# Kernel optimization log

Hardware: AMD Instinct MI355X
Metric: run time of the kernel (lower is better)

## Reference

```python
import jax, jax.numpy as jnp
import numpy as np

B, L, K = 4, 1024, 48
EF, NF, NPE, NRBF, NCLS = 128, 128, 16, 16, 3
MAXREL = 32
EDGE_IN = NPE + NRBF * 25  # 416


def setup_inputs():
    key = jax.random.key(0)
    ks = jax.random.split(key, 8)
    X = jax.random.normal(ks[0], (B, L, 4, 3), jnp.float32)
    mask = jnp.ones((B, L), jnp.float32)
    R_idx = jnp.arange(B * L, dtype=jnp.int64).reshape(B, L)
    chain_labels = jax.random.randint(ks[1], (B, L), 0, 4).astype(jnp.int64)
    membrane_per_residue_labels = jax.random.randint(ks[2], (B, L), 0, NCLS).astype(jnp.int64)
    pe_w = jax.random.normal(ks[3], (2 * MAXREL + 2, NPE), jnp.float32) * 0.05
    pe_b = jax.random.normal(ks[4], (NPE,), jnp.float32) * 0.05
    edge_w = jax.random.normal(ks[5], (EDGE_IN, EF), jnp.float32) * 0.05
    ne_g = jnp.ones((EF,), jnp.float32)
    ne_b = jnp.zeros((EF,), jnp.float32)
    node_w = jax.random.normal(ks[6], (NCLS, NF), jnp.float32) * 0.05
    nn_g = jnp.ones((NF,), jnp.float32)
    nn_b = jnp.zeros((NF,), jnp.float32)
    return {"X": X, "mask": mask, "R_idx": R_idx, "chain_labels": chain_labels,
            "membrane_per_residue_labels": membrane_per_residue_labels,
            "pe_w": pe_w, "pe_b": pe_b, "edge_w": edge_w, "ne_g": ne_g, "ne_b": ne_b,
            "node_w": node_w, "nn_g": nn_g, "nn_b": nn_b}


def _rbf(D):
    mu = jnp.linspace(2.0, 22.0, NRBF)
    sigma = (22.0 - 2.0) / NRBF
    return jnp.exp(-(((D[..., None] - mu) / sigma) ** 2))


def _gather_nb(v, e_idx):
    # v: [B, L, ...] -> [B, L, K, ...] gathered along residue dim
    return jax.vmap(lambda vi, ii: vi[ii])(v, e_idx)


def _ln(x, g, b, eps=1e-5):
    mu = jnp.mean(x, -1, keepdims=True)
    var = jnp.mean((x - mu) ** 2, -1, keepdims=True)
    return (x - mu) / jnp.sqrt(var + eps) * g + b


# 24 atom-pair RBFs after the Ca-Ca (D_neighbors) one, in the original concat order
PAIRS = [("N","N"),("C","C"),("O","O"),("Cb","Cb"),("Ca","N"),("Ca","C"),("Ca","O"),
         ("Ca","Cb"),("N","C"),("N","O"),("N","Cb"),("Cb","C"),("Cb","O"),("O","C"),
         ("N","Ca"),("C","Ca"),("O","Ca"),("Cb","Ca"),("C","N"),("O","N"),("Cb","N"),
         ("C","Cb"),("O","Cb"),("C","O")]


def reference(X, mask, R_idx, chain_labels, membrane_per_residue_labels,
              pe_w, pe_b, edge_w, ne_g, ne_b, node_w, nn_g, nn_b):
    Na, Ca, Cc, Oo = X[:, :, 0], X[:, :, 1], X[:, :, 2], X[:, :, 3]
    bvec = Ca - Na
    cvec = Cc - Ca
    avec = jnp.cross(bvec, cvec)
    Cb = -0.58273431 * avec + 0.56802827 * bvec - 0.54067466 * cvec + Ca
    coords = {"N": Na, "Ca": Ca, "C": Cc, "O": Oo, "Cb": Cb}

    # masked Ca-Ca distances + kNN (single NxN pass)
    mask2 = mask[:, :, None] * mask[:, None, :]
    dX = Ca[:, :, None, :] - Ca[:, None, :, :]
    D = mask2 * jnp.sqrt(jnp.sum(dX ** 2, -1) + 1e-6)
    D_max = jnp.max(D, -1, keepdims=True)
    D_adj = D + (1.0 - mask2) * D_max
    negD, E_idx = jax.lax.top_k(-D_adj, K)
    D_neighbors = -negD  # [B, L, K]

    # gather neighbor coords once, compute the 25 RBF features on N*K pairs only
    nb = {n: _gather_nb(v, E_idx) for n, v in coords.items()}  # [B, L, K, 3]
    rbf_list = [_rbf(D_neighbors)]
    for an, bn in PAIRS:
        d = jnp.sqrt(jnp.sum((coords[an][:, :, None, :] - nb[bn]) ** 2, -1) + 1e-6)
        rbf_list.append(_rbf(d))
    RBF_all = jnp.concatenate(rbf_list, -1)  # [B, L, K, 400]

    # positional encodings on gathered offsets / chain equality
    off = R_idx[:, :, None] - _gather_nb(R_idx, E_idx)           # [B, L, K]
    E_chains = (chain_labels[:, :, None] == _gather_nb(chain_labels, E_idx)).astype(jnp.int32)
    d = jnp.clip(off + MAXREL, 0, 2 * MAXREL).astype(jnp.int32) * E_chains + (1 - E_chains) * (2 * MAXREL + 1)
    d1h = jax.nn.one_hot(d, 2 * MAXREL + 2, dtype=jnp.float32)
    E_pos = d1h @ pe_w + pe_b                                     # [B, L, K, 16]

    E = jnp.concatenate([E_pos, RBF_all], -1) @ edge_w            # [B, L, K, 128]
    E = _ln(E, ne_g, ne_b)

    C1h = jax.nn.one_hot(membrane_per_residue_labels, NCLS, dtype=jnp.float32)
    V = _ln(C1h @ node_w, nn_g, nn_b)                             # [B, L, 128]
    return V, E, E_idx
```

## Files before the change

### kernel.cpp

```cpp
#include <hip/hip_runtime.h>
#include <math.h>

#define B_ 4
#define L_ 1024
#define K_ 48
#define EF_ 128
#define NF_ 128
#define NPE_ 16
#define NRBF_ 16
#define MAXREL_ 32
#define EDGE_IN_ 416

#define V_SIZE   (B_*L_*NF_)
#define E_OFF    (V_SIZE)
#define E_SIZE   (B_*L_*K_*EF_)
#define EIDX_OFF (E_OFF + E_SIZE)

#define XH4_STRIDE 136

typedef __attribute__((ext_vector_type(8))) short bf16x8;
typedef __attribute__((ext_vector_type(4))) float f32x4;
typedef __attribute__((ext_vector_type(4))) unsigned u32x4;

__device__ const int PA_[25] = {1, 0,2,3,4, 1,1,1,1, 0,0,0, 4,4, 3, 0,2,3,4, 2,3,4, 2,3, 2};
__device__ const int PB_[25] = {1, 0,2,3,4, 0,2,3,4, 2,3,4, 2,3, 2, 1,1,1,1, 0,0,0, 4,4, 3};

__device__ __forceinline__ unsigned short f2bf(float f){
    unsigned u = __float_as_uint(f);
    unsigned r = u + 0x7fffu + ((u >> 16) & 1u);
    return (unsigned short)(r >> 16);
}

__device__ __forceinline__ float pair_dist(const float* sAI, const float (*sAJ)[16], int e, int g2) {
    float dx = sAI[PA_[g2]*3+0] - sAJ[e][PB_[g2]*3+0];
    float dy = sAI[PA_[g2]*3+1] - sAJ[e][PB_[g2]*3+1];
    float dz = sAI[PA_[g2]*3+2] - sAJ[e][PB_[g2]*3+2];
    return sqrtf(dx*dx + dy*dy + dz*dz + 1e-6f);
}

__device__ __forceinline__ void rbf16(unsigned short* dst, float dist) {
    float t = 0.8f * dist - 1.6f;
    unsigned pk[8];
    #pragma unroll
    for (int rr = 0; rr < 8; ++rr) {
        float v0 = __expf(-t * t); t -= 1.06666672f;
        float v1 = __expf(-t * t); t -= 1.06666672f;
        asm("v_cvt_pk_bf16_f32 %0, %1, %2" : "=v"(pk[rr]) : "v"(v0), "v"(v1));
    }
    u32x4 w0 = {pk[0], pk[1], pk[2], pk[3]};
    u32x4 w1 = {pk[4], pk[5], pk[6], pk[7]};
    *(u32x4*)dst = w0;
    *(u32x4*)(dst + 8) = w1;
}

template<int NG, int GF, int CB>
__device__ __forceinline__ void rbf_quarter(unsigned short* xh, const float* sAI,
                                            const float (*sAJ)[16], int tid) {
    for (int idx = tid; idx < K_ * NG; idx += 256) {
        int e = idx / NG, g = idx - e * NG;
        rbf16(&xh[e * XH4_STRIDE + CB + g * 16], pair_dist(sAI, sAJ, e, GF + g));
    }
}

template<int NKS, int KB>
__device__ __forceinline__ void mfma_quarter(f32x4 (&acc)[3][2], const unsigned short* xh,
                                             const unsigned short* w0p, const unsigned short* w1p,
                                             int lr, int lg) {
    #pragma unroll
    for (int ks = 0; ks < NKS; ++ks) {
        int k0 = ks * 32;
        bf16x8 a0, a1, a2, wb0, wb1;
        wb0 = *(const bf16x8*)(w0p + KB + k0);
        wb1 = *(const bf16x8*)(w1p + KB + k0);
        a0 = *(const bf16x8*)&xh[(lr)      * XH4_STRIDE + k0 + lg*8];
        a1 = *(const bf16x8*)&xh[(16 + lr) * XH4_STRIDE + k0 + lg*8];
        a2 = *(const bf16x8*)&xh[(32 + lr) * XH4_STRIDE + k0 + lg*8];
        acc[0][0] = __builtin_amdgcn_mfma_f32_16x16x32_bf16(a0, wb0, acc[0][0], 0, 0, 0);
        acc[0][1] = __builtin_amdgcn_mfma_f32_16x16x32_bf16(a0, wb1, acc[0][1], 0, 0, 0);
        acc[1][0] = __builtin_amdgcn_mfma_f32_16x16x32_bf16(a1, wb0, acc[1][0], 0, 0, 0);
        acc[1][1] = __builtin_amdgcn_mfma_f32_16x16x32_bf16(a1, wb1, acc[1][1], 0, 0, 0);
        acc[2][0] = __builtin_amdgcn_mfma_f32_16x16x32_bf16(a2, wb0, acc[2][0], 0, 0, 0);
        acc[2][1] = __builtin_amdgcn_mfma_f32_16x16x32_bf16(a2, wb1, acc[2][1], 0, 0, 0);
    }
}

__global__ __launch_bounds__(256) void wprep_kernel(const float* __restrict__ w,
                                                    unsigned short* __restrict__ wt)
{
    int idx = blockIdx.x * 256 + threadIdx.x;
    if (idx >= EDGE_IN_ * EF_) return;
    int f = idx & 127;
    int k = idx >> 7;
    wt[f * EDGE_IN_ + k] = f2bf(w[k * EF_ + f]);
}

__global__ __launch_bounds__(128) void v_kernel(const int* __restrict__ labels,
                                                const float* __restrict__ node_w,
                                                const float* __restrict__ g,
                                                const float* __restrict__ bb,
                                                float* __restrict__ out)
{
    int gi = blockIdx.x;
    int f  = threadIdx.x;
    int lbl = labels[gi];
    float v = node_w[lbl*NF_ + f];

    __shared__ float red[2];
    __shared__ float red2[2];
    float s = v;
    #pragma unroll
    for (int m = 1; m < 64; m <<= 1) s += __shfl_xor(s, m, 64);
    if ((f & 63) == 0) red[f >> 6] = s;
    __syncthreads();
    float mu = (red[0] + red[1]) * (1.0f / NF_);
    float d = v - mu;
    float s2 = d * d;
    #pragma unroll
    for (int m = 1; m < 64; m <<= 1) s2 += __shfl_xor(s2, m, 64);
    if ((f & 63) == 0) red2[f >> 6] = s2;
    __syncthreads();
    float var = (red2[0] + red2[1]) * (1.0f / NF_);
    out[gi*NF_ + f] = d * rsqrtf(var + 1e-5f) * g[f] + bb[f];
}

__global__ __launch_bounds__(256, 7) void fused_kernel(const float* __restrict__ X,
                                                   const float* __restrict__ mask,
                                                   const int* __restrict__ Ridx,
                                                   const int* __restrict__ chains,
                                                   const float* __restrict__ pe_w,
                                                   const float* __restrict__ pe_b,
                                                   const unsigned short* __restrict__ wt,
                                                   const float* __restrict__ ne_g,
                                                   const float* __restrict__ ne_b,
                                                   float* __restrict__ out)
{
    __shared__ __align__(16) unsigned char sBuf[16384];
    __shared__ __align__(16) unsigned char sAux[1536];
    __shared__ float sAI[16];
    __shared__ float sAJ[K_][16];
    __shared__ int   sJ[K_];
    __shared__ int   sDpos[K_];

    float* sCa = (float*)sBuf;
    float* sM  = (float*)(sBuf + 12288);
    unsigned short* xh = (unsigned short*)sBuf;

    unsigned long long* cand = (unsigned long long*)sAux;
    unsigned* hist   = (unsigned*)(sAux + 384);
    float*    wmax   = (float*)(sAux + 1408);
    int*      sSelBin= (int*)(sAux + 1424);
    unsigned* sSelLo = (unsigned*)(sAux + 1428);
    unsigned* sCnt   = (unsigned*)(sAux + 1432);
    float* stats  = (float*)sAux;
    float* stats2 = (float*)(sAux + 768);

    int tid = threadIdx.x;
    int gi  = blockIdx.x;
    int b   = gi >> 10;
    int i   = gi & (L_ - 1);

    for (int idx = tid; idx < L_ * 3; idx += 256) {
        int j = idx / 3, d = idx - j * 3;
        sCa[idx] = X[(((size_t)((b << 10) + j)) * 4 + 1) * 3 + d];
    }
    for (int j = tid; j < L_; j += 256) sM[j] = mask[(b << 10) + j];
    if (tid == 0) *sCnt = 0;
    __syncthreads();

    float cx = sCa[i*3+0], cy = sCa[i*3+1], cz = sCa[i*3+2];
    float mi = sM[i];

    float dist4[4], m2r[4];
    float lmax = 0.0f;
    #pragma unroll
    for (int q = 0; q < 4; ++q) {
        int j = tid + q * 256;
        float dx = cx - sCa[j*3+0];
        float dy = cy - sCa[j*3+1];
        float dz = cz - sCa[j*3+2];
        float dist = sqrtf(dx*dx + dy*dy + dz*dz + 1e-6f);
        float m2 = mi * sM[j];
        dist4[q] = dist; m2r[q] = m2;
        lmax = fmaxf(lmax, m2 * dist);
    }
    #pragma unroll
    for (int m = 1; m < 64; m <<= 1) lmax = fmaxf(lmax, __shfl_xor(lmax, m, 64));
    if ((tid & 63) == 0) wmax[tid >> 6] = lmax;
    __syncthreads();
    float Dmax = fmaxf(fmaxf(wmax[0], wmax[1]), fmaxf(wmax[2], wmax[3]));

    unsigned long long key[4];
    bool act[4];
    #pragma unroll
    for (int q = 0; q < 4; ++q) {
        int j = tid + q * 256;
        float Dadj = m2r[q] * dist4[q] + (1.0f - m2r[q]) * Dmax;
        key[q] = (((unsigned long long)__float_as_uint(Dadj)) << 32) | (unsigned)j;
        act[q] = true;
    }

    unsigned r = K_ - 1;
    unsigned long long T = 0;
    const int shifts[6] = {56, 48, 40, 32, 8, 0};
    #pragma unroll 1
    for (int p = 0; p < 6; ++p) {
        int sh = shifts[p];
        hist[tid] = 0;
        __syncthreads();
        #pragma unroll
        for (int q = 0; q < 4; ++q)
            if (act[q]) atomicAdd(&hist[(unsigned)((key[q] >> sh) & 255ULL)], 1u);
        __syncthreads();
        if (tid < 64) {
            unsigned b0 = hist[tid*4+0], b1 = hist[tid*4+1], b2 = hist[tid*4+2], b3 = hist[tid*4+3];
            unsigned s0 = b0, s1 = s0 + b1, s2 = s1 + b2, s3 = s2 + b3;
            unsigned s = s3;
            #pragma unroll
            for (int m = 1; m < 64; m <<= 1) {
                unsigned o = __shfl_up(s, m, 64);
                if (tid >= m) s += o;
            }
            unsigned base = s - s3;
            hist[tid*4+0] = base + s0;
            hist[tid*4+1] = base + s1;
            hist[tid*4+2] = base + s2;
            hist[tid*4+3] = base + s3;
        }
        __syncthreads();
        unsigned lo = (tid == 0) ? 0u : hist[tid - 1];
        unsigned hi = hist[tid];
        if (r >= lo && r < hi) { *sSelBin = tid; *sSelLo = lo; }
        __syncthreads();
        int bsel = *sSelBin;
        r -= *sSelLo;
        T |= ((unsigned long long)(unsigned)bsel) << sh;
        #pragma unroll
        for (int q = 0; q < 4; ++q)
            act[q] = act[q] && ((unsigned)((key[q] >> sh) & 255ULL) == (unsigned)bsel);
        __syncthreads();
    }

    #pragma unroll
    for (int q = 0; q < 4; ++q)
        if (key[q] <= T) {
            unsigned pos = atomicAdd(sCnt, 1u);
            cand[pos] = key[q];
        }
    __syncthreads();

    if (tid < 64) {
        unsigned long long k64 = (tid < K_) ? cand[tid] : 0xffffffffffffffffULL;
        #pragma unroll
        for (unsigned kk = 2; kk <= 64; kk <<= 1) {
            #pragma unroll
            for (unsigned jj = kk >> 1; jj > 0; jj >>= 1) {
                unsigned long long o = __shfl_xor(k64, jj, 64);
                bool lower = (tid & jj) == 0;
                bool asc   = (tid & kk) == 0;
                unsigned long long mn = (k64 < o) ? k64 : o;
                unsigned long long mx = (k64 < o) ? o : k64;
                k64 = (lower == asc) ? mn : mx;
            }
        }
        if (tid < K_) {
            int j = (int)(unsigned)(k64 & 0xffffffffULL);
            sJ[tid] = j;
            out[EIDX_OFF + (size_t)gi * K_ + tid] = (float)j;
        }
    }
    __syncthreads();

    if (tid < K_ + 1) {
        int rr = (tid < K_) ? sJ[tid] : i;
        const float* xr = X + ((size_t)((b << 10) + rr)) * 12;
        float n0=xr[0],  n1=xr[1],  n2=xr[2];
        float a0=xr[3],  a1=xr[4],  a2=xr[5];
        float c0=xr[6],  c1=xr[7],  c2=xr[8];
        float o0=xr[9],  o1=xr[10], o2=xr[11];
        float bx=a0-n0, by=a1-n1, bz=a2-n2;
        float vx=c0-a0, vy=c1-a1, vz=c2-a2;
        float ax = by*vz - bz*vy;
        float ay = bz*vx - bx*vz;
        float az = bx*vy - by*vx;
        float cb0 = -0.58273431f*ax + 0.56802827f*bx - 0.54067466f*vx + a0;
        float cb1 = -0.58273431f*ay + 0.56802827f*by - 0.54067466f*vy + a1;
        float cb2 = -0.58273431f*az + 0.56802827f*bz - 0.54067466f*vz + a2;
        float* dst = (tid < K_) ? &sAJ[tid][0] : &sAI[0];
        dst[0]=n0;  dst[1]=n1;  dst[2]=n2;
        dst[3]=a0;  dst[4]=a1;  dst[5]=a2;
        dst[6]=c0;  dst[7]=c1;  dst[8]=c2;
        dst[9]=o0;  dst[10]=o1; dst[11]=o2;
        dst[12]=cb0; dst[13]=cb1; dst[14]=cb2;
    }
    if (tid >= 64 && tid < 64 + K_) {
        int e = tid - 64;
        int j = sJ[e];
        int off  = Ridx[gi] - Ridx[(b << 10) + j];
        int same = (chains[gi] == chains[(b << 10) + j]);
        int dcl = off + MAXREL_;
        dcl = dcl < 0 ? 0 : (dcl > 2*MAXREL_ ? 2*MAXREL_ : dcl);
        sDpos[e] = same ? dcl : (2*MAXREL_ + 1);
    }
    __syncthreads();

    const int wv = tid >> 6;
    const int ln = tid & 63;
    const int lr = ln & 15;
    const int lg = ln >> 4;

    f32x4 acc[3][2];
    #pragma unroll
    for (int rf = 0; rf < 3; ++rf)
        #pragma unroll
        for (int cf = 0; cf < 2; ++cf)
            acc[rf][cf] = (f32x4){0.0f, 0.0f, 0.0f, 0.0f};

    const unsigned short* wbase0 = wt + (size_t)(wv*32 + lr) * EDGE_IN_ + lg*8;
    const unsigned short* wbase1 = wt + (size_t)(wv*32 + 16 + lr) * EDGE_IN_ + lg*8;

    #pragma unroll
    for (int p = 0; p < 2; ++p) {
        int idx = tid + p * 256;
        if (idx < 384) {
            int e = idx >> 3, cc = (idx & 7) * 2;
            int dp = sDpos[e];
            float v0 = pe_w[dp*NPE_ + cc]     + pe_b[cc];
            float v1 = pe_w[dp*NPE_ + cc + 1] + pe_b[cc + 1];
            unsigned pk;
            asm("v_cvt_pk_bf16_f32 %0, %1, %2" : "=v"(pk) : "v"(v0), "v"(v1));
            *(unsigned*)&xh[e * XH4_STRIDE + cc] = pk;
        }
    }
    rbf_quarter<7, 0, 16>(xh, sAI, sAJ, tid);
    __syncthreads();
    mfma_quarter<4, 0>(acc, xh, wbase0, wbase1, lr, lg);
    __syncthreads();
    rbf_quarter<6, 7, 0>(xh, sAI, sAJ, tid);
    __syncthreads();
    mfma_quarter<3, 128>(acc, xh, wbase0, wbase1, lr, lg);
    __syncthreads();
    rbf_quarter<6, 13, 0>(xh, sAI, sAJ, tid);
    __syncthreads();
    mfma_quarter<3, 224>(acc, xh, wbase0, wbase1, lr, lg);
    __syncthreads();
    rbf_quarter<6, 19, 0>(xh, sAI, sAJ, tid);
    __syncthreads();
    mfma_quarter<3, 320>(acc, xh, wbase0, wbase1, lr, lg);

    #pragma unroll
    for (int rf = 0; rf < 3; ++rf)
        #pragma unroll
        for (int r4 = 0; r4 < 4; ++r4) {
            float v0 = acc[rf][0][r4], v1 = acc[rf][1][r4];
            float s  = v0 + v1;
            float s2 = v0*v0 + v1*v1;
            #pragma unroll
            for (int m = 1; m < 16; m <<= 1) {
                s  += __shfl_xor(s,  m, 64);
                s2 += __shfl_xor(s2, m, 64);
            }
            if (lr == 0) {
                int row = rf*16 + lg*4 + r4;
                stats [wv*K_ + row] = s;
                stats2[wv*K_ + row] = s2;
            }
        }
    __syncthreads();

    int colg = wv*32 + lr;
    float gv0 = ne_g[colg],      bv0 = ne_b[colg];
    float gv1 = ne_g[colg + 16], bv1 = ne_b[colg + 16];

    #pragma unroll
    for (int rf = 0; rf < 3; ++rf)
        #pragma unroll
        for (int r4 = 0; r4 < 4; ++r4) {
            int row = rf*16 + lg*4 + r4;
            float sum = stats [row] + stats [K_ + row] + stats [2*K_ + row] + stats [3*K_ + row];
            float sq  = stats2[row] + stats2[K_ + row] + stats2[2*K_ + row] + stats2[3*K_ + row];
            float mu   = sum * (1.0f / 128.0f);
            float var  = sq * (1.0f / 128.0f) - mu * mu;
            float rstd = rsqrtf(var + 1e-5f);
            float* dst = out + E_OFF + (size_t)(gi * K_ + row) * EF_ + colg;
            __builtin_nontemporal_store((acc[rf][0][r4] - mu) * rstd * gv0 + bv0, dst);
            __builtin_nontemporal_store((acc[rf][1][r4] - mu) * rstd * gv1 + bv1, dst + 16);
        }
}

extern "C" void kernel_launch(void* const* d_in, const int* in_sizes, int n_in,
                              void* d_out, int out_size, void* d_ws, size_t ws_size,
                              hipStream_t stream)
{
    const float* X      = (const float*)d_in[0];
    const float* mask   = (const float*)d_in[1];
    const int*   Ridx   = (const int*)d_in[2];
    const int*   chains = (const int*)d_in[3];
    const int*   memb   = (const int*)d_in[4];
    const float* pe_w   = (const float*)d_in[5];
    const float* pe_b   = (const float*)d_in[6];
    const float* edge_w = (const float*)d_in[7];
    const float* ne_g   = (const float*)d_in[8];
    const float* ne_b   = (const float*)d_in[9];
    const float* node_w = (const float*)d_in[10];
    const float* nn_g   = (const float*)d_in[11];
    const float* nn_b   = (const float*)d_in[12];
    float* out = (float*)d_out;

    unsigned short* wt = (unsigned short*)d_ws;

    wprep_kernel<<<(EDGE_IN_*EF_ + 255)/256, 256, 0, stream>>>(edge_w, wt);
    v_kernel<<<B_*L_, 128, 0, stream>>>(memb, node_w, nn_g, nn_b, out);
    fused_kernel<<<B_*L_, 256, 0, stream>>>(X, mask, Ridx, chains, pe_w, pe_b,
                                            wt, ne_g, ne_b, out);
}
```

Before: 110.0 us.

## Single-pass 12-bit histogram top-K select and two-half RBF/MFMA staging

```diff
diff --git a/kernel.cpp b/kernel.cpp
--- a/kernel.cpp
+++ b/kernel.cpp
@@ -16,7 +16,7 @@
 #define E_SIZE   (B_*L_*K_*EF_)
 #define EIDX_OFF (E_OFF + E_SIZE)
 
-#define XH4_STRIDE 136
+#define XH_STRIDE 232
 
 typedef __attribute__((ext_vector_type(8))) short bf16x8;
 typedef __attribute__((ext_vector_type(4))) float f32x4;
@@ -53,28 +53,19 @@
     *(u32x4*)(dst + 8) = w1;
 }
 
-template<int NG, int GF, int CB>
-__device__ __forceinline__ void rbf_quarter(unsigned short* xh, const float* sAI,
-                                            const float (*sAJ)[16], int tid) {
-    for (int idx = tid; idx < K_ * NG; idx += 256) {
-        int e = idx / NG, g = idx - e * NG;
-        rbf16(&xh[e * XH4_STRIDE + CB + g * 16], pair_dist(sAI, sAJ, e, GF + g));
-    }
-}
-
 template<int NKS, int KB>
-__device__ __forceinline__ void mfma_quarter(f32x4 (&acc)[3][2], const unsigned short* xh,
-                                             const unsigned short* w0p, const unsigned short* w1p,
-                                             int lr, int lg) {
+__device__ __forceinline__ void mfma_half(f32x4 (&acc)[3][2], const unsigned short* xh,
+                                          const unsigned short* w0p, const unsigned short* w1p,
+                                          int lr, int lg) {
     #pragma unroll
     for (int ks = 0; ks < NKS; ++ks) {
         int k0 = ks * 32;
         bf16x8 a0, a1, a2, wb0, wb1;
         wb0 = *(const bf16x8*)(w0p + KB + k0);
         wb1 = *(const bf16x8*)(w1p + KB + k0);
-        a0 = *(const bf16x8*)&xh[(lr)      * XH4_STRIDE + k0 + lg*8];
-        a1 = *(const bf16x8*)&xh[(16 + lr) * XH4_STRIDE + k0 + lg*8];
-        a2 = *(const bf16x8*)&xh[(32 + lr) * XH4_STRIDE + k0 + lg*8];
+        a0 = *(const bf16x8*)&xh[(lr)      * XH_STRIDE + k0 + lg*8];
+        a1 = *(const bf16x8*)&xh[(16 + lr) * XH_STRIDE + k0 + lg*8];
+        a2 = *(const bf16x8*)&xh[(32 + lr) * XH_STRIDE + k0 + lg*8];
         acc[0][0] = __builtin_amdgcn_mfma_f32_16x16x32_bf16(a0, wb0, acc[0][0], 0, 0, 0);
         acc[0][1] = __builtin_amdgcn_mfma_f32_16x16x32_bf16(a0, wb1, acc[0][1], 0, 0, 0);
         acc[1][0] = __builtin_amdgcn_mfma_f32_16x16x32_bf16(a1, wb0, acc[1][0], 0, 0, 0);
@@ -123,7 +114,7 @@
     out[gi*NF_ + f] = d * rsqrtf(var + 1e-5f) * g[f] + bb[f];
 }
 
-__global__ __launch_bounds__(256, 7) void fused_kernel(const float* __restrict__ X,
+__global__ __launch_bounds__(256, 5) void fused_kernel(const float* __restrict__ X,
                                                    const float* __restrict__ mask,
                                                    const int* __restrict__ Ridx,
                                                    const int* __restrict__ chains,
@@ -134,25 +125,24 @@
                                                    const float* __restrict__ ne_b,
                                                    float* __restrict__ out)
 {
-    __shared__ __align__(16) unsigned char sBuf[16384];
-    __shared__ __align__(16) unsigned char sAux[1536];
+    __shared__ __align__(16) unsigned char sBuf[K_ * XH_STRIDE * 2];
     __shared__ float sAI[16];
     __shared__ float sAJ[K_][16];
     __shared__ int   sJ[K_];
     __shared__ int   sDpos[K_];
+    __shared__ unsigned long long cand[64];
+    __shared__ float stats [4 * K_];
+    __shared__ float stats2[4 * K_];
+    __shared__ float wmax[4];
+    __shared__ unsigned wsum[4];
+    __shared__ int sSelBin;
+    __shared__ unsigned sSelLo, sSelCnt, sCnt;
+    __shared__ unsigned long long sTkey;
 
     float* sCa = (float*)sBuf;
     float* sM  = (float*)(sBuf + 12288);
+    unsigned* hist32 = (unsigned*)sBuf;
     unsigned short* xh = (unsigned short*)sBuf;
-
-    unsigned long long* cand = (unsigned long long*)sAux;
-    unsigned* hist   = (unsigned*)(sAux + 384);
-    float*    wmax   = (float*)(sAux + 1408);
-    int*      sSelBin= (int*)(sAux + 1424);
-    unsigned* sSelLo = (unsigned*)(sAux + 1428);
-    unsigned* sCnt   = (unsigned*)(sAux + 1432);
-    float* stats  = (float*)sAux;
-    float* stats2 = (float*)(sAux + 768);
 
     int tid = threadIdx.x;
     int gi  = blockIdx.x;
@@ -164,7 +154,6 @@
         sCa[idx] = X[(((size_t)((b << 10) + j)) * 4 + 1) * 3 + d];
     }
     for (int j = tid; j < L_; j += 256) sM[j] = mask[(b << 10) + j];
-    if (tid == 0) *sCnt = 0;
     __syncthreads();
 
     float cx = sCa[i*3+0], cy = sCa[i*3+1], cz = sCa[i*3+2];
@@ -190,60 +179,131 @@
     float Dmax = fmaxf(fmaxf(wmax[0], wmax[1]), fmaxf(wmax[2], wmax[3]));
 
     unsigned long long key[4];
-    bool act[4];
     #pragma unroll
     for (int q = 0; q < 4; ++q) {
         int j = tid + q * 256;
         float Dadj = m2r[q] * dist4[q] + (1.0f - m2r[q]) * Dmax;
         key[q] = (((unsigned long long)__float_as_uint(Dadj)) << 32) | (unsigned)j;
-        act[q] = true;
-    }
-
-    unsigned r = K_ - 1;
-    unsigned long long T = 0;
-    const int shifts[6] = {56, 48, 40, 32, 8, 0};
-    #pragma unroll 1
-    for (int p = 0; p < 6; ++p) {
-        int sh = shifts[p];
-        hist[tid] = 0;
+    }
+
+    for (int k = tid; k < 4096; k += 256) hist32[k] = 0;
+    if (tid == 0) sCnt = 0;
+    __syncthreads();
+    #pragma unroll
+    for (int q = 0; q < 4; ++q)
+        atomicAdd(&hist32[(unsigned)(key[q] >> 51) & 0xFFFu], 1u);
+    __syncthreads();
+
+    u32x4 h4[4];
+    #pragma unroll
+    for (int k = 0; k < 4; ++k) h4[k] = *(u32x4*)&hist32[tid*16 + k*4];
+    unsigned loc[16], tot = 0;
+    #pragma unroll
+    for (int k = 0; k < 16; ++k) { tot += h4[k>>2][k&3]; loc[k] = tot; }
+    unsigned ws = tot;
+    #pragma unroll
+    for (int m = 1; m < 64; m <<= 1) {
+        unsigned o = __shfl_up(ws, m, 64);
+        if ((tid & 63) >= m) ws += o;
+    }
+    if ((tid & 63) == 63) wsum[tid >> 6] = ws;
+    __syncthreads();
+    unsigned base = ws - tot;
+    for (int w = 0; w < (tid >> 6); ++w) base += wsum[w];
+    unsigned lo_t = base;
+    #pragma unroll
+    for (int k = 0; k < 16; ++k) {
+        unsigned hi_t = base + loc[k];
+        if (47u >= lo_t && 47u < hi_t) { sSelBin = tid*16 + k; sSelLo = lo_t; sSelCnt = hi_t - lo_t; }
+        lo_t = hi_t;
+    }
+    __syncthreads();
+    unsigned bsel = (unsigned)sSelBin, lo = sSelLo, c = sSelCnt;
+    unsigned long long T;
+
+    if (c == 1) {
+        #pragma unroll
+        for (int q = 0; q < 4; ++q)
+            if (((unsigned)(key[q] >> 51) & 0xFFFu) == bsel) sTkey = key[q];
         __syncthreads();
+        T = sTkey;
+    } else if (c <= 64) {
         #pragma unroll
         for (int q = 0; q < 4; ++q)
-            if (act[q]) atomicAdd(&hist[(unsigned)((key[q] >> sh) & 255ULL)], 1u);
+            if (((unsigned)(key[q] >> 51) & 0xFFFu) == bsel) {
+                unsigned pos = atomicAdd(&sCnt, 1u);
+                cand[pos] = key[q];
+            }
         __syncthreads();
         if (tid < 64) {
-            unsigned b0 = hist[tid*4+0], b1 = hist[tid*4+1], b2 = hist[tid*4+2], b3 = hist[tid*4+3];
-            unsigned s0 = b0, s1 = s0 + b1, s2 = s1 + b2, s3 = s2 + b3;
-            unsigned s = s3;
+            unsigned long long k64 = (tid < (int)c) ? cand[tid] : 0xffffffffffffffffULL;
             #pragma unroll
-            for (int m = 1; m < 64; m <<= 1) {
-                unsigned o = __shfl_up(s, m, 64);
-                if (tid >= m) s += o;
-            }
-            unsigned base = s - s3;
-            hist[tid*4+0] = base + s0;
-            hist[tid*4+1] = base + s1;
-            hist[tid*4+2] = base + s2;
-            hist[tid*4+3] = base + s3;
-        }
+            for (unsigned kk = 2; kk <= 64; kk <<= 1) {
+                #pragma unroll
+                for (unsigned jj = kk >> 1; jj > 0; jj >>= 1) {
+                    unsigned long long o = __shfl_xor(k64, jj, 64);
+                    bool lower = (tid & jj) == 0;
+                    bool asc   = (tid & kk) == 0;
+                    unsigned long long mn = (k64 < o) ? k64 : o;
+                    unsigned long long mx = (k64 < o) ? o : k64;
+                    k64 = (lower == asc) ? mn : mx;
+                }
+            }
+            if (tid == (int)(47u - lo)) sTkey = k64;
+        }
+        if (tid == 0) sCnt = 0;
         __syncthreads();
-        unsigned lo = (tid == 0) ? 0u : hist[tid - 1];
-        unsigned hi = hist[tid];
-        if (r >= lo && r < hi) { *sSelBin = tid; *sSelLo = lo; }
-        __syncthreads();
-        int bsel = *sSelBin;
-        r -= *sSelLo;
-        T |= ((unsigned long long)(unsigned)bsel) << sh;
-        #pragma unroll
-        for (int q = 0; q < 4; ++q)
-            act[q] = act[q] && ((unsigned)((key[q] >> sh) & 255ULL) == (unsigned)bsel);
+        T = sTkey;
+    } else {
+        bool act[4] = {true, true, true, true};
+        unsigned r = K_ - 1;
+        T = 0;
+        const int shifts[6] = {56, 48, 40, 32, 8, 0};
+        #pragma unroll 1
+        for (int p = 0; p < 6; ++p) {
+            int sh = shifts[p];
+            hist32[tid] = 0;
+            __syncthreads();
+            #pragma unroll
+            for (int q = 0; q < 4; ++q)
+                if (act[q]) atomicAdd(&hist32[(unsigned)((key[q] >> sh) & 255ULL)], 1u);
+            __syncthreads();
+            if (tid < 64) {
+                unsigned b0 = hist32[tid*4+0], b1 = hist32[tid*4+1], b2 = hist32[tid*4+2], b3 = hist32[tid*4+3];
+                unsigned s0 = b0, s1 = s0 + b1, s2 = s1 + b2, s3 = s2 + b3;
+                unsigned s = s3;
+                #pragma unroll
+                for (int m = 1; m < 64; m <<= 1) {
+                    unsigned o = __shfl_up(s, m, 64);
+                    if (tid >= m) s += o;
+                }
+                unsigned bse = s - s3;
+                hist32[tid*4+0] = bse + s0;
+                hist32[tid*4+1] = bse + s1;
+                hist32[tid*4+2] = bse + s2;
+                hist32[tid*4+3] = bse + s3;
+            }
+            __syncthreads();
+            unsigned lo2 = (tid == 0) ? 0u : hist32[tid - 1];
+            unsigned hi2 = hist32[tid];
+            if (r >= lo2 && r < hi2) { sSelBin = tid; sSelLo = lo2; }
+            __syncthreads();
+            int bs2 = sSelBin;
+            r -= sSelLo;
+            T |= ((unsigned long long)(unsigned)bs2) << sh;
+            #pragma unroll
+            for (int q = 0; q < 4; ++q)
+                act[q] = act[q] && ((unsigned)((key[q] >> sh) & 255ULL) == (unsigned)bs2);
+            __syncthreads();
+        }
+        if (tid == 0) sCnt = 0;
         __syncthreads();
     }
 
     #pragma unroll
     for (int q = 0; q < 4; ++q)
         if (key[q] <= T) {
-            unsigned pos = atomicAdd(sCnt, 1u);
+            unsigned pos = atomicAdd(&sCnt, 1u);
             cand[pos] = key[q];
         }
     __syncthreads();
@@ -328,24 +388,30 @@
             float v1 = pe_w[dp*NPE_ + cc + 1] + pe_b[cc + 1];
             unsigned pk;
             asm("v_cvt_pk_bf16_f32 %0, %1, %2" : "=v"(pk) : "v"(v0), "v"(v1));
-            *(unsigned*)&xh[e * XH4_STRIDE + cc] = pk;
-        }
-    }
-    rbf_quarter<7, 0, 16>(xh, sAI, sAJ, tid);
-    __syncthreads();
-    mfma_quarter<4, 0>(acc, xh, wbase0, wbase1, lr, lg);
-    __syncthreads();
-    rbf_quarter<6, 7, 0>(xh, sAI, sAJ, tid);
-    __syncthreads();
-    mfma_quarter<3, 128>(acc, xh, wbase0, wbase1, lr, lg);
-    __syncthreads();
-    rbf_quarter<6, 13, 0>(xh, sAI, sAJ, tid);
-    __syncthreads();
-    mfma_quarter<3, 224>(acc, xh, wbase0, wbase1, lr, lg);
-    __syncthreads();
-    rbf_quarter<6, 19, 0>(xh, sAI, sAJ, tid);
-    __syncthreads();
-    mfma_quarter<3, 320>(acc, xh, wbase0, wbase1, lr, lg);
+            *(unsigned*)&xh[e * XH_STRIDE + cc] = pk;
+        }
+    }
+    #pragma unroll
+    for (int p = 0; p < 3; ++p) {
+        int idx = tid + p * 256;
+        if (idx < 624) {
+            int e = idx / 13, g = idx - e * 13;
+            rbf16(&xh[e * XH_STRIDE + NPE_ + g * 16], pair_dist(sAI, sAJ, e, g));
+        }
+    }
+    __syncthreads();
+    mfma_half<7, 0>(acc, xh, wbase0, wbase1, lr, lg);
+    __syncthreads();
+    #pragma unroll
+    for (int p = 0; p < 3; ++p) {
+        int idx = tid + p * 256;
+        if (idx < 576) {
+            int e = idx / 12, g = 13 + (idx - e * 12);
+            rbf16(&xh[e * XH_STRIDE + (g - 13) * 16], pair_dist(sAI, sAJ, e, g));
+        }
+    }
+    __syncthreads();
+    mfma_half<6, 224>(acc, xh, wbase0, wbase1, lr, lg);
 
     #pragma unroll
     for (int rf = 0; rf < 3; ++rf)
```

New measurement: 100.8 us. -8.4%, faster.
